# Optimization experiments

Measured on AMD Instinct MI355X. Metric: run time of the kernel, lower is better.

The kernel has to match this reference:

```python
import jax, jax.numpy as jnp
import numpy as np

N, D, C = 4096, 2048, 8192
NUM_IDS = 256
MARGIN = 0.3
LABEL_SMOOTHING = 0.1


def setup_inputs() -> dict:
    key = jax.random.key(0)
    k1, k2, k3 = jax.random.split(key, 3)
    embeddings = jax.random.normal(k1, (N, D), dtype=jnp.float32)
    pred_ids = jax.random.normal(k2, (N, C), dtype=jnp.float32)
    target_ids = jax.random.randint(k3, (N,), 0, NUM_IDS, dtype=jnp.int64)
    return {"embeddings": embeddings, "pred_ids": pred_ids, "target_ids": target_ids}


def _euclidean_dist(x, y):
    xx = jnp.sum(x * x, axis=1, keepdims=True)            # [N,1]
    yy = jnp.sum(y * y, axis=1, keepdims=True).T          # [1,N]
    d2 = xx + yy - 2.0 * (x @ y.T)
    return jnp.sqrt(jnp.maximum(d2, 1e-12))


def _cross_entropy_ls(logits, targets, eps):
    # label-smoothed CE, mean over batch
    logp = jax.nn.log_softmax(logits, axis=-1)
    n_cls = logits.shape[-1]
    nll = -jnp.take_along_axis(logp, targets[:, None], axis=1)[:, 0]
    smooth = -jnp.mean(logp, axis=-1)
    return jnp.mean((1.0 - eps) * nll + eps * smooth)


def reference(embeddings, pred_ids, target_ids):
    # ID loss: cross entropy with label smoothing
    id_loss = _cross_entropy_ls(pred_ids, target_ids, LABEL_SMOOTHING)

    # Triplet loss with batch-hard mining
    dist = _euclidean_dist(embeddings, embeddings)        # [N,N]
    pos_mask = target_ids[:, None] == target_ids[None, :] # includes diagonal (as in original)
    neg_inf = jnp.float32(-jnp.inf)
    pos_inf = jnp.float32(jnp.inf)
    dist_ap = jnp.max(jnp.where(pos_mask, dist, neg_inf), axis=1)  # hardest positive
    dist_an = jnp.min(jnp.where(pos_mask, pos_inf, dist), axis=1)  # hardest negative

    # MarginRankingLoss with y=1: mean(relu(dist_ap - dist_an + margin))
    tri_loss = jnp.mean(jnp.maximum(dist_ap - dist_an + MARGIN, 0.0))

    return (id_loss, tri_loss, dist_ap, dist_an)
```

## Files before the change

### kernel.cpp

```cpp
#include <hip/hip_runtime.h>
#include <hip/hip_bf16.h>

typedef unsigned short u16;
typedef unsigned int u32;
typedef __attribute__((ext_vector_type(8))) __bf16 bf16x8;
typedef __attribute__((ext_vector_type(4))) float f32x4;

#define NROW 4096
#define DDIM 2048
#define NCLS 8192
#define MARGIN 0.3f
#define EPS_LS 0.1f
#define FLT_MAX_ 3.402823466e+38f

#define GLOBAL_AS __attribute__((address_space(1)))
#define LDS_AS __attribute__((address_space(3)))

__device__ __forceinline__ void gload_lds16(const void* g, void* l) {
    __builtin_amdgcn_global_load_lds((const GLOBAL_AS u32*)g, (LDS_AS u32*)l, 16, 0, 0);
}

__device__ __forceinline__ u16 f2bf(float f) {
    u32 b = __float_as_uint(f);
    u32 r = (b + 0x7FFFu + ((b >> 16) & 1u)) >> 16;
    return (u16)r;
}

__global__ __launch_bounds__(256) void prep_kernel(
    const float* __restrict__ emb, u16* __restrict__ e16,
    float* __restrict__ xx, int* __restrict__ ap, int* __restrict__ an)
{
    int row = blockIdx.x, tid = threadIdx.x;
    const float4* p = (const float4*)(emb + (size_t)row * DDIM);
    float4 a = p[tid * 2], b = p[tid * 2 + 1];
    float s = a.x*a.x + a.y*a.y + a.z*a.z + a.w*a.w
            + b.x*b.x + b.y*b.y + b.z*b.z + b.w*b.w;

    uint4 pk;
    pk.x = (u32)f2bf(a.x) | ((u32)f2bf(a.y) << 16);
    pk.y = (u32)f2bf(a.z) | ((u32)f2bf(a.w) << 16);
    pk.z = (u32)f2bf(b.x) | ((u32)f2bf(b.y) << 16);
    pk.w = (u32)f2bf(b.z) | ((u32)f2bf(b.w) << 16);
    *(uint4*)&e16[(size_t)row * DDIM + tid * 8] = pk;

    #pragma unroll
    for (int o = 1; o < 64; o <<= 1) s += __shfl_xor(s, o);
    __shared__ float sred[4];
    if ((tid & 63) == 0) sred[tid >> 6] = s;
    __syncthreads();
    if (tid == 0) {
        xx[row] = sred[0] + sred[1] + sred[2] + sred[3];
        ap[row] = 0x80000000;
        an[row] = 0x7FFFFFFF;
    }
}

__global__ __launch_bounds__(256) void ce_kernel(
    const float* __restrict__ pred, const int* __restrict__ tgt,
    float* __restrict__ out)
{
    int row = blockIdx.x, tid = threadIdx.x;
    const float4* p = (const float4*)(pred + (size_t)row * NCLS);
    float4 v[8];
    #pragma unroll
    for (int i = 0; i < 8; ++i) v[i] = p[tid + i * 256];

    float mx = -FLT_MAX_, sm = 0.f;
    #pragma unroll
    for (int i = 0; i < 8; ++i) {
        mx = fmaxf(mx, fmaxf(fmaxf(v[i].x, v[i].y), fmaxf(v[i].z, v[i].w)));
        sm += v[i].x + v[i].y + v[i].z + v[i].w;
    }
    #pragma unroll
    for (int o = 1; o < 64; o <<= 1) {
        mx = fmaxf(mx, __shfl_xor(mx, o));
        sm += __shfl_xor(sm, o);
    }
    __shared__ float smx[4], ssm[4], sse[4];
    int w = tid >> 6;
    if ((tid & 63) == 0) { smx[w] = mx; ssm[w] = sm; }
    __syncthreads();
    mx = fmaxf(fmaxf(smx[0], smx[1]), fmaxf(smx[2], smx[3]));
    sm = ssm[0] + ssm[1] + ssm[2] + ssm[3];

    float es = 0.f;
    #pragma unroll
    for (int i = 0; i < 8; ++i) {
        es += expf(v[i].x - mx) + expf(v[i].y - mx)
            + expf(v[i].z - mx) + expf(v[i].w - mx);
    }
    #pragma unroll
    for (int o = 1; o < 64; o <<= 1) es += __shfl_xor(es, o);
    if ((tid & 63) == 0) sse[w] = es;
    __syncthreads();
    if (tid == 0) {
        es = sse[0] + sse[1] + sse[2] + sse[3];
        float lse = mx + logf(es);
        int t = tgt[row];
        float lt = pred[(size_t)row * NCLS + t];
        float loss = (1.0f - EPS_LS) * (lse - lt)
                   + EPS_LS * (lse - sm * (1.0f / NCLS));
        atomicAdd(out, loss * (1.0f / NROW));
    }
}

__global__ __launch_bounds__(256) void gram_kernel(
    const u16* __restrict__ e16, const float* __restrict__ xx,
    const int* __restrict__ tg, int* __restrict__ ap, int* __restrict__ an)
{
    __shared__ __align__(16) u16 lsA[128 * 64];
    __shared__ __align__(16) u16 lsB[128 * 64];

    int bid = blockIdx.x;
    int wg  = (bid & 7) * 66 + (bid >> 3);
    int tm = (int)(32.5f - sqrtf(32.5f * 32.5f - 2.0f * (float)wg));
    if (tm < 0) tm = 0;
    while (tm < 31 && (tm + 1) * (65 - (tm + 1)) / 2 <= wg) ++tm;
    while (tm > 0 && tm * (65 - tm) / 2 > wg) --tm;
    int tn = tm + (wg - tm * (65 - tm) / 2);
    int rowBase = tm * 128, colBase = tn * 128;
    bool diag = (tm == tn);

    int tid = threadIdx.x;
    int wid = tid >> 6, lane = tid & 63;
    int wm = wid >> 1, wn = wid & 1;

    f32x4 acc[4][4];
    #pragma unroll
    for (int i = 0; i < 4; ++i)
        #pragma unroll
        for (int j = 0; j < 4; ++j) acc[i][j] = (f32x4){0.f, 0.f, 0.f, 0.f};

    int srow = lane >> 3;
    int sslot = lane & 7;

    for (int kb = 0; kb < DDIM; kb += 64) {
        #pragma unroll
        for (int t = 0; t < 4; ++t) {
            int r0 = (wid * 4 + t) * 8;
            int r  = r0 + srow;
            int gsl = sslot ^ (r & 7);
            const u16* ga = &e16[(size_t)(rowBase + r) * DDIM + kb + gsl * 8];
            gload_lds16(ga, &lsA[r0 * 64]);
            const u16* gb = &e16[(size_t)(colBase + r) * DDIM + kb + gsl * 8];
            gload_lds16(gb, &lsB[r0 * 64]);
        }
        __syncthreads();

        #pragma unroll
        for (int h = 0; h < 2; ++h) {
            bf16x8 af[4], bfr[4];
            #pragma unroll
            for (int fm = 0; fm < 4; ++fm) {
                int row = wm * 64 + fm * 16 + (lane & 15);
                int sl = (h * 4 + (lane >> 4)) ^ (row & 7);
                af[fm] = *(const bf16x8*)&lsA[row * 64 + sl * 8];
            }
            #pragma unroll
            for (int fn = 0; fn < 4; ++fn) {
                int row = wn * 64 + fn * 16 + (lane & 15);
                int sl = (h * 4 + (lane >> 4)) ^ (row & 7);
                bfr[fn] = *(const bf16x8*)&lsB[row * 64 + sl * 8];
            }
            #pragma unroll
            for (int fm = 0; fm < 4; ++fm)
                #pragma unroll
                for (int fn = 0; fn < 4; ++fn)
                    acc[fm][fn] = __builtin_amdgcn_mfma_f32_16x16x32_bf16(
                        af[fm], bfr[fn], acc[fm][fn], 0, 0, 0);
        }
        __syncthreads();
    }

    float xc[4]; int tc[4];
    float capc[4], canc[4];
    #pragma unroll
    for (int fn = 0; fn < 4; ++fn) {
        int gc = colBase + wn * 64 + fn * 16 + (lane & 15);
        xc[fn] = xx[gc];
        tc[fn] = tg[gc];
        capc[fn] = -FLT_MAX_;
        canc[fn] = FLT_MAX_;
    }
    #pragma unroll
    for (int fm = 0; fm < 4; ++fm) {
        #pragma unroll
        for (int reg = 0; reg < 4; ++reg) {
            int gr = rowBase + wm * 64 + fm * 16 + (lane >> 4) * 4 + reg;
            float xr = xx[gr];
            int   tr = tg[gr];
            float cap = -FLT_MAX_, can = FLT_MAX_;
            #pragma unroll
            for (int fn = 0; fn < 4; ++fn) {
                int gc = colBase + wn * 64 + fn * 16 + (lane & 15);
                float d2 = xr + xc[fn] - 2.0f * acc[fm][fn][reg];
                d2 = fmaxf(d2, 0.0f);
                if (gr == gc) d2 = 0.0f;
                bool pos = (tr == tc[fn]);
                if (pos) { cap = fmaxf(cap, d2); capc[fn] = fmaxf(capc[fn], d2); }
                else     { can = fminf(can, d2); canc[fn] = fminf(canc[fn], d2); }
            }
            #pragma unroll
            for (int o = 1; o < 16; o <<= 1) {
                cap = fmaxf(cap, __shfl_xor(cap, o));
                can = fminf(can, __shfl_xor(can, o));
            }
            if ((lane & 15) == 0) {
                atomicMax(&ap[gr], __float_as_int(cap));
                atomicMin(&an[gr], __float_as_int(can));
            }
        }
    }
    if (!diag) {
        #pragma unroll
        for (int fn = 0; fn < 4; ++fn) {
            float cap = capc[fn], can = canc[fn];
            cap = fmaxf(cap, __shfl_xor(cap, 16));
            can = fminf(can, __shfl_xor(can, 16));
            cap = fmaxf(cap, __shfl_xor(cap, 32));
            can = fminf(can, __shfl_xor(can, 32));
            if (lane < 16) {
                int gc = colBase + wn * 64 + fn * 16 + lane;
                atomicMax(&ap[gc], __float_as_int(cap));
                atomicMin(&an[gc], __float_as_int(can));
            }
        }
    }
}

__global__ __launch_bounds__(256) void final_kernel(
    const int* __restrict__ ap, const int* __restrict__ an,
    float* __restrict__ out)
{
    int i = blockIdx.x * 256 + threadIdx.x;
    float a2 = __int_as_float(ap[i]);
    float n2 = __int_as_float(an[i]);
    float av = sqrtf(fmaxf(a2, 1e-12f));
    float nv = sqrtf(fmaxf(n2, 1e-12f));
    out[2 + i] = av;
    out[2 + NROW + i] = nv;
    float t = fmaxf(av - nv + MARGIN, 0.0f);
    #pragma unroll
    for (int o = 1; o < 64; o <<= 1) t += __shfl_xor(t, o);
    __shared__ float sred[4];
    if ((threadIdx.x & 63) == 0) sred[threadIdx.x >> 6] = t;
    __syncthreads();
    if (threadIdx.x == 0)
        atomicAdd(out + 1, (sred[0] + sred[1] + sred[2] + sred[3]) * (1.0f / NROW));
}

extern "C" void kernel_launch(void* const* d_in, const int* in_sizes, int n_in,
                              void* d_out, int out_size, void* d_ws, size_t ws_size,
                              hipStream_t stream)
{
    const float* emb  = (const float*)d_in[0];
    const float* pred = (const float*)d_in[1];
    const int*   tgt  = (const int*)d_in[2];
    float* out = (float*)d_out;

    char* ws = (char*)d_ws;
    u16*   e16 = (u16*)ws;
    float* xx  = (float*)(ws + (size_t)16 * 1024 * 1024);
    int*   ap  = (int*)(ws + (size_t)16 * 1024 * 1024 + 16384);
    int*   an  = (int*)(ws + (size_t)16 * 1024 * 1024 + 32768);

    hipMemsetAsync(d_out, 0, 2 * sizeof(float), stream);
    prep_kernel <<<NROW, 256, 0, stream>>>(emb, e16, xx, ap, an);
    ce_kernel   <<<NROW, 256, 0, stream>>>(pred, tgt, out);
    gram_kernel <<<528, 256, 0, stream>>>(e16, xx, tgt, ap, an);
    final_kernel<<<NROW / 256, 256, 0, stream>>>(ap, an, out);
}
```

Before: 330.4 us.

## Fuse cross-entropy rows into gram kernel and shrink gram tiles to 64x128

Replaces the separate cross-entropy and gram launches with one fused kernel of 5280 blocks. Every fifth block computes a 64x128 upper-triangular tile of the distance matrix, and the other four each handle one cross-entropy row. The aim is to overlap the bandwidth-bound softmax pass with the MFMA-bound gram work and to spread work across more, smaller tiles. In exchange, operand reuse per tile drops and the column-side atomics now also run on diagonal tiles.

```diff
diff --git a/kernel.cpp b/kernel.cpp
--- a/kernel.cpp
+++ b/kernel.cpp
@@ -55,11 +55,11 @@
     }
 }
 
-__global__ __launch_bounds__(256) void ce_kernel(
-    const float* __restrict__ pred, const int* __restrict__ tgt,
-    float* __restrict__ out)
-{
-    int row = blockIdx.x, tid = threadIdx.x;
+__device__ __forceinline__ void ce_block(
+    int row, const float* __restrict__ pred, const int* __restrict__ tgt,
+    float* __restrict__ out, float* smem )
+{
+    int tid = threadIdx.x;
     const float4* p = (const float4*)(pred + (size_t)row * NCLS);
     float4 v[8];
     #pragma unroll
@@ -76,7 +76,7 @@
         mx = fmaxf(mx, __shfl_xor(mx, o));
         sm += __shfl_xor(sm, o);
     }
-    __shared__ float smx[4], ssm[4], sse[4];
+    float* smx = smem; float* ssm = smem + 4; float* sse = smem + 8;
     int w = tid >> 6;
     if ((tid & 63) == 0) { smx[w] = mx; ssm[w] = sm; }
     __syncthreads();
@@ -104,30 +104,45 @@
     }
 }
 
-__global__ __launch_bounds__(256) void gram_kernel(
+__global__ __launch_bounds__(256) void fused_kernel(
     const u16* __restrict__ e16, const float* __restrict__ xx,
-    const int* __restrict__ tg, int* __restrict__ ap, int* __restrict__ an)
-{
-    __shared__ __align__(16) u16 lsA[128 * 64];
+    const int* __restrict__ tg, int* __restrict__ ap, int* __restrict__ an,
+    const float* __restrict__ pred, float* __restrict__ out)
+{
+    __shared__ __align__(16) u16 lsA[64 * 64];
     __shared__ __align__(16) u16 lsB[128 * 64];
+    __shared__ float cered[12];
 
     int bid = blockIdx.x;
-    int wg  = (bid & 7) * 66 + (bid >> 3);
-    int tm = (int)(32.5f - sqrtf(32.5f * 32.5f - 2.0f * (float)wg));
-    if (tm < 0) tm = 0;
-    while (tm < 31 && (tm + 1) * (65 - (tm + 1)) / 2 <= wg) ++tm;
-    while (tm > 0 && tm * (65 - tm) / 2 > wg) --tm;
-    int tn = tm + (wg - tm * (65 - tm) / 2);
-    int rowBase = tm * 128, colBase = tn * 128;
-    bool diag = (tm == tn);
+    int q = bid / 5, rsel = bid - q * 5;
+    if (rsel != 0) {
+        int row = q * 4 + rsel - 1;
+        if (row < NROW) ce_block(row, pred, tg, out, cered);
+        return;
+    }
+
+    int g = q;
+    int wg = ((g * 5) & 7) * 132 + (g >> 3);
+
+    float sq = sqrtf(4225.0f - 4.0f * (float)wg);
+    int m = (int)((65.0f - sq) * 0.5f);
+    if (m < 0) m = 0;
+    if (m > 31) m = 31;
+    while (m > 0 && m * (65 - m) > wg) --m;
+    while (m < 31 && (m + 1) * (64 - m) <= wg) ++m;
+    int off = wg - m * (65 - m);
+    int half = 32 - m;
+    int r = 2 * m + (off >= half ? 1 : 0);
+    int c = m + (off >= half ? off - half : off);
+    int rowBase = r * 64, colBase = c * 128;
 
     int tid = threadIdx.x;
     int wid = tid >> 6, lane = tid & 63;
     int wm = wid >> 1, wn = wid & 1;
 
-    f32x4 acc[4][4];
-    #pragma unroll
-    for (int i = 0; i < 4; ++i)
+    f32x4 acc[2][4];
+    #pragma unroll
+    for (int i = 0; i < 2; ++i)
         #pragma unroll
         for (int j = 0; j < 4; ++j) acc[i][j] = (f32x4){0.f, 0.f, 0.f, 0.f};
 
@@ -136,23 +151,29 @@
 
     for (int kb = 0; kb < DDIM; kb += 64) {
         #pragma unroll
+        for (int t = 0; t < 2; ++t) {
+            int r0 = wid * 16 + t * 8;
+            int rr = r0 + srow;
+            int gsl = sslot ^ (rr & 7);
+            gload_lds16(&e16[(size_t)(rowBase + rr) * DDIM + kb + gsl * 8],
+                        &lsA[r0 * 64]);
+        }
+        #pragma unroll
         for (int t = 0; t < 4; ++t) {
-            int r0 = (wid * 4 + t) * 8;
-            int r  = r0 + srow;
-            int gsl = sslot ^ (r & 7);
-            const u16* ga = &e16[(size_t)(rowBase + r) * DDIM + kb + gsl * 8];
-            gload_lds16(ga, &lsA[r0 * 64]);
-            const u16* gb = &e16[(size_t)(colBase + r) * DDIM + kb + gsl * 8];
-            gload_lds16(gb, &lsB[r0 * 64]);
+            int r0 = wid * 32 + t * 8;
+            int rr = r0 + srow;
+            int gsl = sslot ^ (rr & 7);
+            gload_lds16(&e16[(size_t)(colBase + rr) * DDIM + kb + gsl * 8],
+                        &lsB[r0 * 64]);
         }
         __syncthreads();
 
         #pragma unroll
         for (int h = 0; h < 2; ++h) {
-            bf16x8 af[4], bfr[4];
-            #pragma unroll
-            for (int fm = 0; fm < 4; ++fm) {
-                int row = wm * 64 + fm * 16 + (lane & 15);
+            bf16x8 af[2], bfr[4];
+            #pragma unroll
+            for (int fm = 0; fm < 2; ++fm) {
+                int row = wm * 32 + fm * 16 + (lane & 15);
                 int sl = (h * 4 + (lane >> 4)) ^ (row & 7);
                 af[fm] = *(const bf16x8*)&lsA[row * 64 + sl * 8];
             }
@@ -163,7 +184,7 @@
                 bfr[fn] = *(const bf16x8*)&lsB[row * 64 + sl * 8];
             }
             #pragma unroll
-            for (int fm = 0; fm < 4; ++fm)
+            for (int fm = 0; fm < 2; ++fm)
                 #pragma unroll
                 for (int fn = 0; fn < 4; ++fn)
                     acc[fm][fn] = __builtin_amdgcn_mfma_f32_16x16x32_bf16(
@@ -183,10 +204,10 @@
         canc[fn] = FLT_MAX_;
     }
     #pragma unroll
-    for (int fm = 0; fm < 4; ++fm) {
+    for (int fm = 0; fm < 2; ++fm) {
         #pragma unroll
         for (int reg = 0; reg < 4; ++reg) {
-            int gr = rowBase + wm * 64 + fm * 16 + (lane >> 4) * 4 + reg;
+            int gr = rowBase + wm * 32 + fm * 16 + (lane >> 4) * 4 + reg;
             float xr = xx[gr];
             int   tr = tg[gr];
             float cap = -FLT_MAX_, can = FLT_MAX_;
@@ -211,19 +232,17 @@
             }
         }
     }
-    if (!diag) {
-        #pragma unroll
-        for (int fn = 0; fn < 4; ++fn) {
-            float cap = capc[fn], can = canc[fn];
-            cap = fmaxf(cap, __shfl_xor(cap, 16));
-            can = fminf(can, __shfl_xor(can, 16));
-            cap = fmaxf(cap, __shfl_xor(cap, 32));
-            can = fminf(can, __shfl_xor(can, 32));
-            if (lane < 16) {
-                int gc = colBase + wn * 64 + fn * 16 + lane;
-                atomicMax(&ap[gc], __float_as_int(cap));
-                atomicMin(&an[gc], __float_as_int(can));
-            }
+    #pragma unroll
+    for (int fn = 0; fn < 4; ++fn) {
+        float cap = capc[fn], can = canc[fn];
+        cap = fmaxf(cap, __shfl_xor(cap, 16));
+        can = fminf(can, __shfl_xor(can, 16));
+        cap = fmaxf(cap, __shfl_xor(cap, 32));
+        can = fminf(can, __shfl_xor(can, 32));
+        if (lane < 16) {
+            int gc = colBase + wn * 64 + fn * 16 + lane;
+            atomicMax(&ap[gc], __float_as_int(cap));
+            atomicMin(&an[gc], __float_as_int(can));
         }
     }
 }
@@ -266,7 +285,6 @@
 
     hipMemsetAsync(d_out, 0, 2 * sizeof(float), stream);
     prep_kernel <<<NROW, 256, 0, stream>>>(emb, e16, xx, ap, an);
-    ce_kernel   <<<NROW, 256, 0, stream>>>(pred, tgt, out);
-    gram_kernel <<<528, 256, 0, stream>>>(e16, xx, tgt, ap, an);
+    fused_kernel<<<5280, 256, 0, stream>>>(e16, xx, tgt, ap, an, pred, out);
     final_kernel<<<NROW / 256, 256, 0, stream>>>(ap, an, out);
 }
```

After: 294.7 us. 10.8% less time.

## Fuse cross-entropy rows into the gram kernel grid to overlap compute and bandwidth

Applied to the files above, without the earlier changes.

The separate cross-entropy kernel is merged into the gram kernel as one launch of 4752 blocks. One block in nine runs a gram tile and the other eight each handle one CE row, so the bandwidth-bound softmax work can overlap the MFMA-bound distance tiles. This saves a launch and the serialization between the two kernels. In exchange, the fused blocks carry the gram kernel's LDS footprint (32KB) even for CE rows, which may lower occupancy for the CE work, and gram tiles are dispersed through the grid.

```diff
diff --git a/kernel.cpp b/kernel.cpp
--- a/kernel.cpp
+++ b/kernel.cpp
@@ -55,11 +55,11 @@
     }
 }
 
-__global__ __launch_bounds__(256) void ce_kernel(
-    const float* __restrict__ pred, const int* __restrict__ tgt,
-    float* __restrict__ out)
-{
-    int row = blockIdx.x, tid = threadIdx.x;
+__device__ __forceinline__ void ce_block(
+    int row, const float* __restrict__ pred, const int* __restrict__ tgt,
+    float* __restrict__ out, float* smem )
+{
+    int tid = threadIdx.x;
     const float4* p = (const float4*)(pred + (size_t)row * NCLS);
     float4 v[8];
     #pragma unroll
@@ -76,7 +76,7 @@
         mx = fmaxf(mx, __shfl_xor(mx, o));
         sm += __shfl_xor(sm, o);
     }
-    __shared__ float smx[4], ssm[4], sse[4];
+    float* smx = smem; float* ssm = smem + 4; float* sse = smem + 8;
     int w = tid >> 6;
     if ((tid & 63) == 0) { smx[w] = mx; ssm[w] = sm; }
     __syncthreads();
@@ -104,15 +104,28 @@
     }
 }
 
-__global__ __launch_bounds__(256) void gram_kernel(
+__global__ __launch_bounds__(256) void fused_kernel(
     const u16* __restrict__ e16, const float* __restrict__ xx,
-    const int* __restrict__ tg, int* __restrict__ ap, int* __restrict__ an)
+    const int* __restrict__ tg, int* __restrict__ ap, int* __restrict__ an,
+    const float* __restrict__ pred, float* __restrict__ out)
 {
     __shared__ __align__(16) u16 lsA[128 * 64];
     __shared__ __align__(16) u16 lsB[128 * 64];
+    __shared__ float cered[12];
 
     int bid = blockIdx.x;
-    int wg  = (bid & 7) * 66 + (bid >> 3);
+    int tid = threadIdx.x;
+    int q = bid / 9, rsel = bid - q * 9;
+
+    if (rsel != 0) {
+        int row = q * 8 + rsel - 1;
+        if (row < NROW) ce_block(row, pred, tg, out, cered);
+        return;
+    }
+
+    int g = q;
+    int wg = (g & 7) * 66 + (g >> 3);
+
     int tm = (int)(32.5f - sqrtf(32.5f * 32.5f - 2.0f * (float)wg));
     if (tm < 0) tm = 0;
     while (tm < 31 && (tm + 1) * (65 - (tm + 1)) / 2 <= wg) ++tm;
@@ -121,7 +134,6 @@
     int rowBase = tm * 128, colBase = tn * 128;
     bool diag = (tm == tn);
 
-    int tid = threadIdx.x;
     int wid = tid >> 6, lane = tid & 63;
     int wm = wid >> 1, wn = wid & 1;
 
@@ -140,10 +152,10 @@
             int r0 = (wid * 4 + t) * 8;
             int r  = r0 + srow;
             int gsl = sslot ^ (r & 7);
-            const u16* ga = &e16[(size_t)(rowBase + r) * DDIM + kb + gsl * 8];
-            gload_lds16(ga, &lsA[r0 * 64]);
-            const u16* gb = &e16[(size_t)(colBase + r) * DDIM + kb + gsl * 8];
-            gload_lds16(gb, &lsB[r0 * 64]);
+            gload_lds16(&e16[(size_t)(rowBase + r) * DDIM + kb + gsl * 8],
+                        &lsA[r0 * 64]);
+            gload_lds16(&e16[(size_t)(colBase + r) * DDIM + kb + gsl * 8],
+                        &lsB[r0 * 64]);
         }
         __syncthreads();
 
@@ -266,7 +278,6 @@
 
     hipMemsetAsync(d_out, 0, 2 * sizeof(float), stream);
     prep_kernel <<<NROW, 256, 0, stream>>>(emb, e16, xx, ap, an);
-    ce_kernel   <<<NROW, 256, 0, stream>>>(pred, tgt, out);
-    gram_kernel <<<528, 256, 0, stream>>>(e16, xx, tgt, ap, an);
+    fused_kernel<<<4752, 256, 0, stream>>>(e16, xx, tgt, ap, an, pred, out);
     final_kernel<<<NROW / 256, 256, 0, stream>>>(ap, an, out);
 }
```

New measurement: 300.3 us. -9.1%, faster.
